# Kernel tuning notes

Measured on AMD Instinct MI355X. Metric: run time of the kernel, lower is better.

Reference implementation:

```python
import jax, jax.numpy as jnp
import numpy as np

B, S, E, H = 1, 4096, 768, 12
DH = E // H  # 64


def setup_inputs() -> dict:
    key = jax.random.key(0)
    ks = jax.random.split(key, 4)
    x = jax.random.normal(ks[0], (B, S, E), dtype=jnp.float32)
    mask = jnp.tril(jnp.ones((S, S), dtype=bool))  # causal mask, broadcast over B,H
    w_qkv = jax.random.normal(ks[1], (3 * E, E), dtype=jnp.float32) * 0.02
    b_qkv = jnp.zeros((3 * E,), dtype=jnp.float32)
    w_out = jax.random.normal(ks[2], (E, E), dtype=jnp.float32) * 0.02
    b_out = jnp.zeros((E,), dtype=jnp.float32)
    return {"x": x, "mask": mask, "w_qkv": w_qkv, "b_qkv": b_qkv,
            "w_out": w_out, "b_out": b_out}


def reference(x, mask, w_qkv, b_qkv, w_out, b_out):
    b, s, e = x.shape
    # qkv projection: torch Linear is x @ W^T + b
    qkv = x @ w_qkv.T + b_qkv                      # [B,S,3E]
    q, k, v = jnp.split(qkv, 3, axis=-1)           # each [B,S,E]
    def heads(t):
        return t.reshape(b, s, H, DH).transpose(0, 2, 1, 3)  # [B,H,S,Dh]
    q, k, v = heads(q), heads(k), heads(v)
    # NOTE: original module does NOT scale by 1/sqrt(head_dim)
    scores = jnp.einsum('bhqd,bhkd->bhqk', q, k)   # [B,H,S,S]
    scores = jnp.where(mask, scores, -jnp.inf)     # masked_fill(mask==0, -inf)
    probs = jax.nn.softmax(scores, axis=-1)        # dropout=0 (eval)
    attn = jnp.einsum('bhqk,bhkd->bhqd', probs, v) # [B,H,S,Dh]
    attn = attn.transpose(0, 2, 1, 3).reshape(b, s, e)
    return attn @ w_out.T + b_out
```

## Files before the change

### kernel.cpp

```cpp
#include <hip/hip_runtime.h>
#include <hip/hip_bf16.h>

#define S_LEN 4096
#define EMB   768
#define NH    12
#define DH    64
#define NCHUNK 4
#define CKL2   10

#define LOG2E 1.44269504088896f

#define NEG_BIG (-1e30f)

#define EXP2F(x) __builtin_amdgcn_exp2f(x)

using bf16x8 = __attribute__((ext_vector_type(8))) short;
using bf16x4 = __attribute__((ext_vector_type(4))) short;
using f32x4  = __attribute__((ext_vector_type(4))) float;

__device__ __forceinline__ short f2bf(float f) {
    __hip_bfloat16 h = __float2bfloat16(f);
    short s; __builtin_memcpy(&s, &h, 2); return s;
}
__device__ __forceinline__ float bf2f(short s) {
    __hip_bfloat16 h; __builtin_memcpy(&h, &s, 2);
    return __bfloat162float(h);
}

__device__ __forceinline__ unsigned pack_bf16_rh(float a, float b) {
    unsigned ua, ub;
    __builtin_memcpy(&ua, &a, 4);
    __builtin_memcpy(&ub, &b, 4);
    return __builtin_amdgcn_perm(ub + 0x8000u, ua + 0x8000u, 0x07060302u);
}

__device__ __forceinline__ void gld_lds16(const void* g, void* l) {
    __builtin_amdgcn_global_load_lds(
        (const __attribute__((address_space(1))) unsigned int*)g,
        (__attribute__((address_space(3))) unsigned int*)l, 16, 0, 0);
}

__device__ __forceinline__ void cvt8(const float* s, short* d, int i) {
    const float4 a = ((const float4*)s)[i * 2];
    const float4 b = ((const float4*)s)[i * 2 + 1];
    bf16x8 o;
    o[0] = f2bf(a.x); o[1] = f2bf(a.y); o[2] = f2bf(a.z); o[3] = f2bf(a.w);
    o[4] = f2bf(b.x); o[5] = f2bf(b.y); o[6] = f2bf(b.z); o[7] = f2bf(b.w);
    ((bf16x8*)d)[i] = o;
}

__global__ __launch_bounds__(256) void cvt_bf16(
    const float* __restrict__ s, short* __restrict__ d, int n8)
{
    const int i = blockIdx.x * 256 + threadIdx.x;
    if (i < n8) cvt8(s, d, i);
}

__global__ __launch_bounds__(256) void cvt3_bf16(
    const float* __restrict__ x,  short* __restrict__ xb,  int n8x,
    const float* __restrict__ wq, short* __restrict__ wqb, int n8q,
    const float* __restrict__ wo, short* __restrict__ wob, int n8o)
{
    int i = blockIdx.x * 256 + threadIdx.x;
    if (i < n8x) { cvt8(x, xb, i); return; }
    i -= n8x;
    if (i < n8q) { cvt8(wq, wqb, i); return; }
    i -= n8q;
    if (i < n8o) cvt8(wo, wob, i);
}

__global__ __launch_bounds__(256) void qkv_gemm(
    const short* __restrict__ Xb, const short* __restrict__ Wb,
    const float* __restrict__ Bias,
    short* __restrict__ Qw, short* __restrict__ Kw, short* __restrict__ Vt)
{
    __shared__ __align__(16) short SMEM[2 * 128 * 64];
    short* As = SMEM;
    short* Bs = SMEM + 128 * 64;

    const int m0 = blockIdx.x * 128;
    const int n0 = blockIdx.y * 128;
    const int t = threadIdx.x;
    const int lane = t & 63, wave = t >> 6;
    const int quad = lane >> 4, l16 = lane & 15;
    const int wm = (wave >> 1) * 64, wn = (wave & 1) * 64;
    const int srow = lane >> 3, scol = (lane & 7) * 8;

    f32x4 acc[4][4] = {};

    for (int k0 = 0; k0 < EMB; k0 += 64) {
        #pragma unroll
        for (int qd = 0; qd < 4; qd++) {
            const int chunk = wave * 4 + qd;
            const int row = chunk * 8 + srow;
            gld_lds16(&Xb[(size_t)(m0 + row) * EMB + k0 + scol], &As[chunk * 512]);
            gld_lds16(&Wb[(size_t)(n0 + row) * EMB + k0 + scol], &Bs[chunk * 512]);
        }
        __syncthreads();

        #pragma unroll
        for (int kb = 0; kb < 2; kb++) {
            bf16x8 af[4], bfr[4];
            #pragma unroll
            for (int i = 0; i < 4; i++)
                af[i] = *(const bf16x8*)&As[(wm + i * 16 + l16) * 64 + kb * 32 + quad * 8];
            #pragma unroll
            for (int j = 0; j < 4; j++)
                bfr[j] = *(const bf16x8*)&Bs[(wn + j * 16 + l16) * 64 + kb * 32 + quad * 8];
            #pragma unroll
            for (int i = 0; i < 4; i++)
                #pragma unroll
                for (int j = 0; j < 4; j++)
                    acc[i][j] = __builtin_amdgcn_mfma_f32_16x16x32_bf16(
                        af[i], bfr[j], acc[i][j], 0, 0, 0);
        }
        __syncthreads();
    }

    const int part = n0 / EMB;

    if (part < 2) {
        const float qs = (part == 0) ? LOG2E : 1.0f;
        #pragma unroll
        for (int j = 0; j < 4; j++) {
            const int n = n0 + wn + j * 16 + l16;
            const float bias = Bias[n];
            const int r768 = n % EMB;
            const int h = r768 >> 6, d = r768 & 63;
            short* dst = (part == 0) ? Qw : Kw;
            #pragma unroll
            for (int i = 0; i < 4; i++)
                #pragma unroll
                for (int r = 0; r < 4; r++) {
                    const int m = m0 + wm + i * 16 + quad * 4 + r;
                    dst[((size_t)h * S_LEN + m) * DH + d] =
                        f2bf((acc[i][j][r] + bias) * qs);
                }
        }
    } else {
        #pragma unroll
        for (int j = 0; j < 4; j++) {
            const int nl = wn + j * 16 + l16;
            const float bias = Bias[n0 + nl];
            #pragma unroll
            for (int i = 0; i < 4; i++) {
                short4 v;
                v.x = f2bf(acc[i][j][0] + bias);
                v.y = f2bf(acc[i][j][1] + bias);
                v.z = f2bf(acc[i][j][2] + bias);
                v.w = f2bf(acc[i][j][3] + bias);
                *(short4*)&SMEM[nl * 128 + wm + i * 16 + quad * 4] = v;
            }
        }
        __syncthreads();
        const int vrow0 = n0 - 2 * EMB;
        #pragma unroll
        for (int c = t; c < 2048; c += 256) {
            const int row = c >> 4, off = (c & 15) * 8;
            *(bf16x8*)&Vt[(size_t)(vrow0 + row) * S_LEN + m0 + off] =
                *(const bf16x8*)&SMEM[row * 128 + off];
        }
    }
}

__global__ __launch_bounds__(256, 4) void flash_partial(
    const short* __restrict__ Qw, const short* __restrict__ Kw,
    const short* __restrict__ Vt,
    short* __restrict__ Opart, float* __restrict__ Mpart,
    float* __restrict__ Lpart)
{
    const int qt = (gridDim.x - 1) - blockIdx.x;
    const int h  = blockIdx.y;
    const int kc = blockIdx.z;
    const int q0  = qt * 64;
    const int ks0 = kc << CKL2;
    if (ks0 > q0) return;
    const int KIT = (1 << CKL2) / 128;
    const int T  = q0 >> 7;
    const int nk = min(KIT, T - KIT * kc + 1);

    __shared__ __align__(16) short SMEM[128 * 64 + 64 * 128];
    short* Ks = SMEM;
    short* Vs = SMEM + 128 * 64;

    const int t = threadIdx.x;
    const int lane = t & 63, wave = t >> 6;
    const int quad = lane >> 4, l16 = lane & 15;
    const int qw0 = q0 + wave * 16;
    const int swk = (l16 & 7) << 4;
    const int swv = l16 << 4;

    const short* Kh = Kw + (size_t)h * S_LEN * DH;
    const short* Vh = Vt + (size_t)h * DH * S_LEN;

    const int krow = lane >> 3;
    const int kcol = ((lane & 7) ^ krow) << 3;
    const int vrow = lane >> 4;
    const int vsc  = lane & 15;

    bf16x8 qf[2];
    #pragma unroll
    for (int kb = 0; kb < 2; kb++)
        qf[kb] = *(const bf16x8*)
            &Qw[((size_t)h * S_LEN + qw0 + l16) * DH + kb * 32 + quad * 8];

    float m_i = NEG_BIG, l_i = 0.f;
    f32x4 o_acc[4] = {};

    for (int kt = 0; kt < nk; kt++) {
        const int k0 = ks0 + kt * 128;

        __syncthreads();
        #pragma unroll
        for (int i = 0; i < 4; i++) {
            const int ck = wave * 4 + i;
            const int rk = ck * 8 + krow;
            gld_lds16(&Kh[(size_t)(k0 + rk) * DH + kcol], &Ks[ck * 512]);
            const int rv = ck * 4 + vrow;
            const int vcol = (vsc ^ (rv & 15)) << 3;
            gld_lds16(&Vh[(size_t)rv * S_LEN + k0 + vcol], &Vs[ck * 512]);
        }
        __syncthreads();

        const bool maskn = (k0 + 127 > q0);
        #pragma unroll
        for (int sub = 0; sub < 2; sub++) {
            const int kbase = k0 + sub * 64;
            if (maskn && kbase > qw0 + 15) continue;

            f32x4 sfT[4] = {};
            __builtin_amdgcn_s_setprio(1);
            #pragma unroll
            for (int bb = 0; bb < 4; bb++) {
                const int row = (sub * 4 + bb) * 16 + l16;
                #pragma unroll
                for (int kb = 0; kb < 2; kb++) {
                    const bf16x8 kf = *(const bf16x8*)((const char*)Ks
                        + row * 128 + ((kb * 64 + quad * 16) ^ swk));
                    sfT[bb] = __builtin_amdgcn_mfma_f32_16x16x32_bf16(
                        kf, qf[kb], sfT[bb], 0, 0, 0);
                }
            }
            __builtin_amdgcn_s_setprio(0);

            const int qg = qw0 + l16;
            if (maskn) {
                #pragma unroll
                for (int bb = 0; bb < 4; bb++)
                    #pragma unroll
                    for (int r = 0; r < 4; r++)
                        if (kbase + bb * 16 + quad * 4 + r > qg)
                            sfT[bb][r] = NEG_BIG;
            }

            float mx = sfT[0][0];
            #pragma unroll
            for (int bb = 0; bb < 4; bb++)
                #pragma unroll
                for (int r = 0; r < 4; r++) mx = fmaxf(mx, sfT[bb][r]);
            mx = fmaxf(mx, __shfl_xor(mx, 16, 64));
            mx = fmaxf(mx, __shfl_xor(mx, 32, 64));
            if (!__all(mx <= m_i + 8.0f)) {
                const float mnew = fmaxf(m_i, mx);
                const float alpha = EXP2F(m_i - mnew);
                m_i = mnew;
                l_i *= alpha;
                #pragma unroll
                for (int db = 0; db < 4; db++) o_acc[db] *= alpha;
            }
            float rs = 0.f;
            #pragma unroll
            for (int bb = 0; bb < 4; bb++)
                #pragma unroll
                for (int r = 0; r < 4; r++) {
                    const float p = EXP2F(sfT[bb][r] - m_i);
                    sfT[bb][r] = p;
                    rs += p;
                }
            rs += __shfl_xor(rs, 16, 64);
            rs += __shfl_xor(rs, 32, 64);
            l_i += rs;

            __builtin_amdgcn_s_setprio(1);
            #pragma unroll
            for (int bp = 0; bp < 2; bp++) {
                int4 pv;
                pv.x = (int)pack_bf16_rh(sfT[2 * bp][0],     sfT[2 * bp][1]);
                pv.y = (int)pack_bf16_rh(sfT[2 * bp][2],     sfT[2 * bp][3]);
                pv.z = (int)pack_bf16_rh(sfT[2 * bp + 1][0], sfT[2 * bp + 1][1]);
                pv.w = (int)pack_bf16_rh(sfT[2 * bp + 1][2], sfT[2 * bp + 1][3]);
                const bf16x8 pf = __builtin_bit_cast(bf16x8, pv);
                const int colb = (sub * 2 + bp) * 64 + quad * 8;
                #pragma unroll
                for (int db = 0; db < 4; db++) {
                    const char* vb = (const char*)Vs + (db * 16 + l16) * 256;
                    const int2 lo2 = *(const int2*)(vb + (colb ^ swv));
                    const int2 hi2 = *(const int2*)(vb + ((colb + 32) ^ swv));
                    int4 vi; vi.x = lo2.x; vi.y = lo2.y; vi.z = hi2.x; vi.w = hi2.y;
                    o_acc[db] = __builtin_amdgcn_mfma_f32_16x16x32_bf16(
                        __builtin_bit_cast(bf16x8, vi), pf, o_acc[db], 0, 0, 0);
                }
            }
            __builtin_amdgcn_s_setprio(0);
        }
    }

    const size_t slab = ((size_t)h * NCHUNK + kc) * S_LEN;

    if (quad == 0) {
        const int q = qw0 + l16;
        Mpart[slab + q] = m_i;
        Lpart[slab + q] = l_i;
    }

    __syncthreads();
    #pragma unroll
    for (int db = 0; db < 4; db++) {
        short4 pk4;
        pk4.x = f2bf(o_acc[db][0]); pk4.y = f2bf(o_acc[db][1]);
        pk4.z = f2bf(o_acc[db][2]); pk4.w = f2bf(o_acc[db][3]);
        *(short4*)&SMEM[(wave * 16 + l16) * 72 + db * 16 + quad * 4] = pk4;
    }
    __syncthreads();
    #pragma unroll
    for (int c = t; c < 512; c += 256) {
        const int row = c >> 3, off = (c & 7) * 8;
        *(bf16x8*)&Opart[(slab + q0 + row) * DH + off] =
            *(const bf16x8*)&SMEM[row * 72 + off];
    }
}

__global__ __launch_bounds__(256) void flash_merge(
    const short* __restrict__ Opart, const float* __restrict__ Mpart,
    const float* __restrict__ Lpart, short* __restrict__ Ctx)
{
    const int row = blockIdx.x * 4 + (threadIdx.x >> 6);
    const int lane = threadIdx.x & 63;
    const int h = row >> 12, q = row & 4095;
    const int nc = (q >> CKL2) + 1;

    float mv[NCHUNK], lv[NCHUNK];
    float M = NEG_BIG;
    #pragma unroll
    for (int c = 0; c < NCHUNK; c++) {
        if (c < nc) {
            mv[c] = Mpart[((size_t)h * NCHUNK + c) * S_LEN + q];
            lv[c] = Lpart[((size_t)h * NCHUNK + c) * S_LEN + q];
            M = fmaxf(M, mv[c]);
        }
    }
    float L = 0.f, O = 0.f;
    #pragma unroll
    for (int c = 0; c < NCHUNK; c++) {
        if (c < nc) {
            const float w = EXP2F(mv[c] - M);
            L += w * lv[c];
            O += w * bf2f(Opart[(((size_t)h * NCHUNK + c) * S_LEN + q) * DH + lane]);
        }
    }
    const float inv = (L > 0.f) ? 1.0f / L : 0.f;
    Ctx[(size_t)q * EMB + h * DH + lane] = f2bf(O * inv);
}

__global__ __launch_bounds__(256) void flash_attn(
    const short* __restrict__ Qw, const short* __restrict__ Kw,
    const short* __restrict__ Vt, short* __restrict__ Ctx)
{
    __shared__ __align__(16) short Ks[128 * 64];
    __shared__ __align__(16) short Vs[64 * 128];
    __shared__ __align__(16) short Ps[4][32 * 128];

    const int h  = blockIdx.y;
    const int qt = (gridDim.x - 1) - blockIdx.x;
    const int q0 = qt * 128;
    const int t = threadIdx.x;
    const int lane = t & 63, wave = t >> 6;
    const int quad = lane >> 4, l16 = lane & 15;
    const int qw0 = q0 + wave * 32;

    bf16x8 qf[2][2];
    #pragma unroll
    for (int i = 0; i < 2; i++)
        #pragma unroll
        for (int kb = 0; kb < 2; kb++)
            qf[i][kb] = *(const bf16x8*)
                &Qw[((size_t)h * S_LEN + qw0 + i * 16 + l16) * DH + kb * 32 + quad * 8];

    float m_i[2][4], l_i[2][4];
    f32x4 o_acc[2][4] = {};
    #pragma unroll
    for (int i = 0; i < 2; i++)
        #pragma unroll
        for (int r = 0; r < 4; r++) { m_i[i][r] = NEG_BIG; l_i[i][r] = 0.f; }

    for (int kt = 0; kt <= qt; kt++) {
        const int k0 = kt * 128;
        __syncthreads();
        for (int c = t; c < 1024; c += 256) {
            const int row = c >> 3, cc = (c & 7) * 8;
            *(bf16x8*)&Ks[row * 64 + cc] =
                *(const bf16x8*)&Kw[((size_t)h * S_LEN + k0 + row) * DH + cc];
        }
        for (int c = t; c < 1024; c += 256) {
            const int row = c >> 4, cc = (c & 15) * 8;
            *(bf16x8*)&Vs[row * 128 + cc] =
                *(const bf16x8*)&Vt[((size_t)h * DH + row) * S_LEN + k0 + cc];
        }
        __syncthreads();

        f32x4 sf[2][8] = {};
        #pragma unroll
        for (int j = 0; j < 8; j++) {
            #pragma unroll
            for (int kb = 0; kb < 2; kb++) {
                const bf16x8 kf = *(const bf16x8*)
                    &Ks[(j * 16 + l16) * 64 + kb * 32 + quad * 8];
                #pragma unroll
                for (int i = 0; i < 2; i++)
                    sf[i][j] = __builtin_amdgcn_mfma_f32_16x16x32_bf16(
                        qf[i][kb], kf, sf[i][j], 0, 0, 0);
            }
        }

        const bool diag = (kt == qt);
        #pragma unroll
        for (int i = 0; i < 2; i++) {
            if (diag) {
                const int qbase = qw0 + i * 16 + quad * 4;
                const int kbase = k0 + l16;
                #pragma unroll
                for (int j = 0; j < 8; j++)
                    #pragma unroll
                    for (int r = 0; r < 4; r++)
                        if (kbase + j * 16 > qbase + r) sf[i][j][r] = NEG_BIG;
            }
            #pragma unroll
            for (int r = 0; r < 4; r++) {
                float mx = sf[i][0][r];
                #pragma unroll
                for (int j = 1; j < 8; j++) mx = fmaxf(mx, sf[i][j][r]);
                #pragma unroll
                for (int off = 1; off < 16; off <<= 1)
                    mx = fmaxf(mx, __shfl_xor(mx, off, 64));
                const float mnew = fmaxf(m_i[i][r], mx);
                const float alpha = EXP2F(m_i[i][r] - mnew);
                m_i[i][r] = mnew;
                float rs = 0.f;
                #pragma unroll
                for (int j = 0; j < 8; j++) {
                    const float p = EXP2F(sf[i][j][r] - mnew);
                    sf[i][j][r] = p;
                    rs += p;
                }
                #pragma unroll
                for (int off = 1; off < 16; off <<= 1)
                    rs += __shfl_xor(rs, off, 64);
                l_i[i][r] = l_i[i][r] * alpha + rs;
                #pragma unroll
                for (int db = 0; db < 4; db++) o_acc[i][db][r] *= alpha;
            }
            #pragma unroll
            for (int j = 0; j < 8; j++)
                #pragma unroll
                for (int r = 0; r < 4; r++)
                    Ps[wave][(i * 16 + quad * 4 + r) * 128 + j * 16 + l16] =
                        f2bf(sf[i][j][r]);
        }

        #pragma unroll
        for (int kb = 0; kb < 4; kb++) {
            bf16x8 pf[2];
            #pragma unroll
            for (int i = 0; i < 2; i++)
                pf[i] = *(const bf16x8*)
                    &Ps[wave][(i * 16 + l16) * 128 + kb * 32 + quad * 8];
            #pragma unroll
            for (int db = 0; db < 4; db++) {
                const bf16x8 vf = *(const bf16x8*)
                    &Vs[(db * 16 + l16) * 128 + kb * 32 + quad * 8];
                #pragma unroll
                for (int i = 0; i < 2; i++)
                    o_acc[i][db] = __builtin_amdgcn_mfma_f32_16x16x32_bf16(
                        pf[i], vf, o_acc[i][db], 0, 0, 0);
            }
        }
    }

    #pragma unroll
    for (int i = 0; i < 2; i++)
        #pragma unroll
        for (int r = 0; r < 4; r++) {
            const float li = l_i[i][r];
            const float inv = (li > 0.f) ? 1.0f / li : 0.f;
            const int m = qw0 + i * 16 + quad * 4 + r;
            #pragma unroll
            for (int db = 0; db < 4; db++) {
                const int d = db * 16 + l16;
                Ctx[(size_t)m * EMB + h * DH + d] = f2bf(o_acc[i][db][r] * inv);
            }
        }
}

__global__ __launch_bounds__(256) void out_gemm(
    const short* __restrict__ A, const short* __restrict__ Wb,
    const float* __restrict__ Bias, float* __restrict__ Out)
{
    __shared__ __align__(16) short As[128 * 64];
    __shared__ __align__(16) short Bs[128 * 64];

    const int m0 = blockIdx.x * 128;
    const int n0 = blockIdx.y * 128;
    const int t = threadIdx.x;
    const int lane = t & 63, wave = t >> 6;
    const int quad = lane >> 4, l16 = lane & 15;
    const int wm = (wave >> 1) * 64, wn = (wave & 1) * 64;
    const int srow = lane >> 3, scol = (lane & 7) * 8;

    f32x4 acc[4][4] = {};

    for (int k0 = 0; k0 < EMB; k0 += 64) {
        #pragma unroll
        for (int qd = 0; qd < 4; qd++) {
            const int chunk = wave * 4 + qd;
            const int row = chunk * 8 + srow;
            gld_lds16(&A [(size_t)(m0 + row) * EMB + k0 + scol], &As[chunk * 512]);
            gld_lds16(&Wb[(size_t)(n0 + row) * EMB + k0 + scol], &Bs[chunk * 512]);
        }
        __syncthreads();

        #pragma unroll
        for (int kb = 0; kb < 2; kb++) {
            bf16x8 af[4], bfr[4];
            #pragma unroll
            for (int i = 0; i < 4; i++)
                af[i] = *(const bf16x8*)&As[(wm + i * 16 + l16) * 64 + kb * 32 + quad * 8];
            #pragma unroll
            for (int j = 0; j < 4; j++)
                bfr[j] = *(const bf16x8*)&Bs[(wn + j * 16 + l16) * 64 + kb * 32 + quad * 8];
            #pragma unroll
            for (int i = 0; i < 4; i++)
                #pragma unroll
                for (int j = 0; j < 4; j++)
                    acc[i][j] = __builtin_amdgcn_mfma_f32_16x16x32_bf16(
                        af[i], bfr[j], acc[i][j], 0, 0, 0);
        }
        __syncthreads();
    }

    #pragma unroll
    for (int j = 0; j < 4; j++) {
        const int n = n0 + wn + j * 16 + l16;
        const float bias = Bias[n];
        #pragma unroll
        for (int i = 0; i < 4; i++)
            #pragma unroll
            for (int r = 0; r < 4; r++) {
                const int m = m0 + wm + i * 16 + quad * 4 + r;
                Out[(size_t)m * EMB + n] = acc[i][j][r] + bias;
            }
    }
}

extern "C" void kernel_launch(void* const* d_in, const int* in_sizes, int n_in,
                              void* d_out, int out_size, void* d_ws, size_t ws_size,
                              hipStream_t stream)
{
    (void)in_sizes; (void)n_in; (void)out_size;
    const float* x     = (const float*)d_in[0];
    const float* w_qkv = (const float*)d_in[2];
    const float* b_qkv = (const float*)d_in[3];
    const float* w_out = (const float*)d_in[4];
    const float* b_out = (const float*)d_in[5];
    float* out = (float*)d_out;

    char* ws = (char*)d_ws;
    const size_t SEG = (size_t)NH * S_LEN * DH * sizeof(short);
    short* Qw  = (short*)(ws);
    short* Kw  = (short*)(ws + SEG);
    short* Vt  = (short*)(ws + 2 * SEG);
    short* Ctx = (short*)(ws + 3 * SEG);
    const size_t OP_OFF = 4 * SEG;
    const size_t OP_SZ  = (size_t)NH * NCHUNK * S_LEN * DH * sizeof(short);
    const size_t ML_SZ  = (size_t)NH * NCHUNK * S_LEN * sizeof(float);
    short* Opart = (short*)(ws + OP_OFF);
    float* Mpart = (float*)(ws + OP_OFF + OP_SZ);
    float* Lpart = (float*)(ws + OP_OFF + OP_SZ + ML_SZ);
    const size_t need = OP_OFF + OP_SZ + 2 * ML_SZ;

    const int XN8 = (S_LEN * EMB) / 8;
    const int WQ8 = (3 * EMB * EMB) / 8;
    const int WO8 = (EMB * EMB) / 8;
    const size_t WO_BYTES = (size_t)EMB * EMB * sizeof(short);
    short* Xb    = (short*)(ws + OP_OFF);
    short* Wqkvb = (short*)(ws + OP_OFF + (size_t)XN8 * 8 * sizeof(short));
    const bool big = ws_size >= need + WO_BYTES;
    short* Woutb = big ? (short*)(ws + need) : (short*)(ws + OP_OFF);

    if (big) {
        const int tot8 = XN8 + WQ8 + WO8;
        cvt3_bf16<<<dim3((tot8 + 255) / 256), 256, 0, stream>>>(
            x, Xb, XN8, w_qkv, Wqkvb, WQ8, w_out, Woutb, WO8);
    } else {
        cvt_bf16<<<dim3((XN8 + 255) / 256), 256, 0, stream>>>(x, Xb, XN8);
        cvt_bf16<<<dim3((WQ8 + 255) / 256), 256, 0, stream>>>(w_qkv, Wqkvb, WQ8);
    }

    qkv_gemm<<<dim3(S_LEN / 128, (3 * EMB) / 128), 256, 0, stream>>>(
        Xb, Wqkvb, b_qkv, Qw, Kw, Vt);

    if (ws_size >= need) {
        flash_partial<<<dim3(S_LEN / 64, NH, NCHUNK), 256, 0, stream>>>(
            Qw, Kw, Vt, Opart, Mpart, Lpart);
        flash_merge<<<dim3(NH * S_LEN / 4), 256, 0, stream>>>(
            Opart, Mpart, Lpart, Ctx);
    } else {
        flash_attn<<<dim3(S_LEN / 128, NH), 256, 0, stream>>>(Qw, Kw, Vt, Ctx);
    }

    if (!big)
        cvt_bf16<<<dim3((WO8 + 255) / 256), 256, 0, stream>>>(w_out, Woutb, WO8);
    out_gemm<<<dim3(S_LEN / 128, EMB / 128), 256, 0, stream>>>(
        Ctx, Woutb, b_out, out);
}
```

Measured before the change: 254.4 us.

## Double-buffer K/V tiles, process full 128-key tile, fold row-sum into MFMA

Adds a two-stage LDS ping-pong so the next K/V tile loads asynchronously while the current one is computed, using explicit vmcnt waits and barriers. The two 64-key sub-iterations are merged into one 128-key softmax step, so the max and rescale work runs once per tile. The softmax row-sum is now produced by an extra MFMA against a ones vector instead of shuffle reductions, and packing uses v_cvt_pk_bf16_f32. LDS doubles and launch bounds drop to 2 waves per SIMD, which lowers occupancy and raises register pressure.

```diff
diff --git a/kernel.cpp b/kernel.cpp
--- a/kernel.cpp
+++ b/kernel.cpp
@@ -32,6 +32,12 @@
     __builtin_memcpy(&ua, &a, 4);
     __builtin_memcpy(&ub, &b, 4);
     return __builtin_amdgcn_perm(ub + 0x8000u, ua + 0x8000u, 0x07060302u);
+}
+
+__device__ __forceinline__ unsigned cvt_pk_bf16(float a, float b) {
+    unsigned r;
+    asm("v_cvt_pk_bf16_f32 %0, %1, %2" : "=v"(r) : "v"(a), "v"(b));
+    return r;
 }
 
 __device__ __forceinline__ void gld_lds16(const void* g, void* l) {
@@ -163,7 +169,7 @@
     }
 }
 
-__global__ __launch_bounds__(256, 4) void flash_partial(
+__global__ __launch_bounds__(256, 2) void flash_partial(
     const short* __restrict__ Qw, const short* __restrict__ Kw,
     const short* __restrict__ Vt,
     short* __restrict__ Opart, float* __restrict__ Mpart,
@@ -179,9 +185,7 @@
     const int T  = q0 >> 7;
     const int nk = min(KIT, T - KIT * kc + 1);
 
-    __shared__ __align__(16) short SMEM[128 * 64 + 64 * 128];
-    short* Ks = SMEM;
-    short* Vs = SMEM + 128 * 64;
+    __shared__ __align__(16) short SMEM[2 * 16384];
 
     const int t = threadIdx.x;
     const int lane = t & 63, wave = t >> 6;
@@ -204,93 +208,118 @@
         qf[kb] = *(const bf16x8*)
             &Qw[((size_t)h * S_LEN + qw0 + l16) * DH + kb * 32 + quad * 8];
 
-    float m_i = NEG_BIG, l_i = 0.f;
-    f32x4 o_acc[4] = {};
-
-    for (int kt = 0; kt < nk; kt++) {
-        const int k0 = ks0 + kt * 128;
-
-        __syncthreads();
+    bf16x8 vfc;
+    {
+        const short o1 = (l16 == 0) ? (short)0x3F80 : (short)0;
+        #pragma unroll
+        for (int c = 0; c < 8; c++) vfc[c] = o1;
+    }
+
+    auto stage = [&](int K0, int p) {
+        short* Ks = SMEM + p * 16384;
+        short* Vs = Ks + 8192;
         #pragma unroll
         for (int i = 0; i < 4; i++) {
             const int ck = wave * 4 + i;
             const int rk = ck * 8 + krow;
-            gld_lds16(&Kh[(size_t)(k0 + rk) * DH + kcol], &Ks[ck * 512]);
+            gld_lds16(&Kh[(size_t)(K0 + rk) * DH + kcol], &Ks[ck * 512]);
             const int rv = ck * 4 + vrow;
             const int vcol = (vsc ^ (rv & 15)) << 3;
-            gld_lds16(&Vh[(size_t)rv * S_LEN + k0 + vcol], &Vs[ck * 512]);
-        }
-        __syncthreads();
+            gld_lds16(&Vh[(size_t)rv * S_LEN + K0 + vcol], &Vs[ck * 512]);
+        }
+    };
+
+    stage(ks0, 0);
+
+    float m_i = NEG_BIG;
+    f32x4 o_acc[5] = {};
+
+    for (int kt = 0; kt < nk; kt++) {
+        const int k0 = ks0 + kt * 128;
+        const int p = kt & 1;
+        const short* Ks = SMEM + p * 16384;
+        const short* Vs = Ks + 8192;
+
+        __builtin_amdgcn_sched_barrier(0);
+        if (kt + 1 < nk) {
+            stage(k0 + 128, p ^ 1);
+            __builtin_amdgcn_sched_barrier(0);
+            asm volatile("s_waitcnt vmcnt(8)" ::: "memory");
+        } else {
+            asm volatile("s_waitcnt vmcnt(0)" ::: "memory");
+        }
+        __builtin_amdgcn_sched_barrier(0);
+        __builtin_amdgcn_s_barrier();
+        __builtin_amdgcn_sched_barrier(0);
 
         const bool maskn = (k0 + 127 > q0);
-        #pragma unroll
-        for (int sub = 0; sub < 2; sub++) {
-            const int kbase = k0 + sub * 64;
-            if (maskn && kbase > qw0 + 15) continue;
-
-            f32x4 sfT[4] = {};
-            __builtin_amdgcn_s_setprio(1);
-            #pragma unroll
-            for (int bb = 0; bb < 4; bb++) {
-                const int row = (sub * 4 + bb) * 16 + l16;
+        const bool do1 = !(maskn && (k0 + 64 > qw0 + 15));
+
+        f32x4 sfT[8];
+        __builtin_amdgcn_s_setprio(1);
+        #pragma unroll
+        for (int j = 0; j < 8; j++) {
+            if (j < 4 || do1) {
+                sfT[j] = f32x4{};
+                const int row = j * 16 + l16;
                 #pragma unroll
                 for (int kb = 0; kb < 2; kb++) {
                     const bf16x8 kf = *(const bf16x8*)((const char*)Ks
                         + row * 128 + ((kb * 64 + quad * 16) ^ swk));
-                    sfT[bb] = __builtin_amdgcn_mfma_f32_16x16x32_bf16(
-                        kf, qf[kb], sfT[bb], 0, 0, 0);
+                    sfT[j] = __builtin_amdgcn_mfma_f32_16x16x32_bf16(
+                        kf, qf[kb], sfT[j], 0, 0, 0);
                 }
             }
-            __builtin_amdgcn_s_setprio(0);
-
-            const int qg = qw0 + l16;
-            if (maskn) {
-                #pragma unroll
-                for (int bb = 0; bb < 4; bb++)
+        }
+        __builtin_amdgcn_s_setprio(0);
+
+        const int qg = qw0 + l16;
+        if (maskn) {
+            #pragma unroll
+            for (int j = 0; j < 8; j++)
+                if (j < 4 || do1) {
                     #pragma unroll
                     for (int r = 0; r < 4; r++)
-                        if (kbase + bb * 16 + quad * 4 + r > qg)
-                            sfT[bb][r] = NEG_BIG;
-            }
-
-            float mx = sfT[0][0];
-            #pragma unroll
-            for (int bb = 0; bb < 4; bb++)
-                #pragma unroll
-                for (int r = 0; r < 4; r++) mx = fmaxf(mx, sfT[bb][r]);
-            mx = fmaxf(mx, __shfl_xor(mx, 16, 64));
-            mx = fmaxf(mx, __shfl_xor(mx, 32, 64));
-            if (!__all(mx <= m_i + 8.0f)) {
-                const float mnew = fmaxf(m_i, mx);
-                const float alpha = EXP2F(m_i - mnew);
-                m_i = mnew;
-                l_i *= alpha;
-                #pragma unroll
-                for (int db = 0; db < 4; db++) o_acc[db] *= alpha;
-            }
-            float rs = 0.f;
-            #pragma unroll
-            for (int bb = 0; bb < 4; bb++)
-                #pragma unroll
-                for (int r = 0; r < 4; r++) {
-                    const float p = EXP2F(sfT[bb][r] - m_i);
-                    sfT[bb][r] = p;
-                    rs += p;
+                        if (k0 + j * 16 + quad * 4 + r > qg)
+                            sfT[j][r] = NEG_BIG;
                 }
-            rs += __shfl_xor(rs, 16, 64);
-            rs += __shfl_xor(rs, 32, 64);
-            l_i += rs;
-
-            __builtin_amdgcn_s_setprio(1);
-            #pragma unroll
-            for (int bp = 0; bp < 2; bp++) {
+        }
+
+        float mx = sfT[0][0];
+        #pragma unroll
+        for (int j = 0; j < 8; j++)
+            if (j < 4 || do1) {
+                #pragma unroll
+                for (int r = 0; r < 4; r++) mx = fmaxf(mx, sfT[j][r]);
+            }
+        mx = fmaxf(mx, __shfl_xor(mx, 16, 64));
+        mx = fmaxf(mx, __shfl_xor(mx, 32, 64));
+        if (!__all(mx <= m_i + 8.0f)) {
+            const float mnew = fmaxf(m_i, mx);
+            const float alpha = EXP2F(m_i - mnew);
+            m_i = mnew;
+            #pragma unroll
+            for (int db = 0; db < 5; db++) o_acc[db] *= alpha;
+        }
+        #pragma unroll
+        for (int j = 0; j < 8; j++)
+            if (j < 4 || do1) {
+                #pragma unroll
+                for (int r = 0; r < 4; r++)
+                    sfT[j][r] = EXP2F(sfT[j][r] - m_i);
+            }
+
+        __builtin_amdgcn_s_setprio(1);
+        #pragma unroll
+        for (int bp = 0; bp < 4; bp++) {
+            if (bp < 2 || do1) {
                 int4 pv;
-                pv.x = (int)pack_bf16_rh(sfT[2 * bp][0],     sfT[2 * bp][1]);
-                pv.y = (int)pack_bf16_rh(sfT[2 * bp][2],     sfT[2 * bp][3]);
-                pv.z = (int)pack_bf16_rh(sfT[2 * bp + 1][0], sfT[2 * bp + 1][1]);
-                pv.w = (int)pack_bf16_rh(sfT[2 * bp + 1][2], sfT[2 * bp + 1][3]);
+                pv.x = (int)cvt_pk_bf16(sfT[2 * bp][0],     sfT[2 * bp][1]);
+                pv.y = (int)cvt_pk_bf16(sfT[2 * bp][2],     sfT[2 * bp][3]);
+                pv.z = (int)cvt_pk_bf16(sfT[2 * bp + 1][0], sfT[2 * bp + 1][1]);
+                pv.w = (int)cvt_pk_bf16(sfT[2 * bp + 1][2], sfT[2 * bp + 1][3]);
                 const bf16x8 pf = __builtin_bit_cast(bf16x8, pv);
-                const int colb = (sub * 2 + bp) * 64 + quad * 8;
+                const int colb = bp * 64 + quad * 8;
                 #pragma unroll
                 for (int db = 0; db < 4; db++) {
                     const char* vb = (const char*)Vs + (db * 16 + l16) * 256;
@@ -300,9 +329,14 @@
                     o_acc[db] = __builtin_amdgcn_mfma_f32_16x16x32_bf16(
                         __builtin_bit_cast(bf16x8, vi), pf, o_acc[db], 0, 0, 0);
                 }
-            }
-            __builtin_amdgcn_s_setprio(0);
-        }
+                o_acc[4] = __builtin_amdgcn_mfma_f32_16x16x32_bf16(
+                    vfc, pf, o_acc[4], 0, 0, 0);
+            }
+        }
+        __builtin_amdgcn_s_setprio(0);
+
+        __builtin_amdgcn_sched_barrier(0);
+        __builtin_amdgcn_s_barrier();
     }
 
     const size_t slab = ((size_t)h * NCHUNK + kc) * S_LEN;
@@ -310,7 +344,7 @@
     if (quad == 0) {
         const int q = qw0 + l16;
         Mpart[slab + q] = m_i;
-        Lpart[slab + q] = l_i;
+        Lpart[slab + q] = o_acc[4][0];
     }
 
     __syncthreads();
```

Result: slower. 265.1 us (+4.2%).

## Process two 16-row query tiles per wave and compute row sums via MFMA

Applied to the files above, without the earlier changes.

Each flash_partial block now covers 128 query rows, with each wave handling 32 rows as two 16-row tiles. Every K/V fragment loaded from LDS is reused across both tiles, which halves K/V staging traffic per query and the grid size. The softmax row sum is computed by an extra MFMA against a ones-column vector instead of shuffle reductions. P is packed to bf16 with a hardware convert instruction in place of the manual round-half perm trick. The costs are more registers (launch bounds drop from 4 to 3 blocks per CU), fewer blocks to fill the GPU, and the risk that the l computed from bf16-rounded P differs slightly from the fp32 sum.

```diff
diff --git a/kernel.cpp b/kernel.cpp
--- a/kernel.cpp
+++ b/kernel.cpp
@@ -27,11 +27,10 @@
     return __bfloat162float(h);
 }
 
-__device__ __forceinline__ unsigned pack_bf16_rh(float a, float b) {
-    unsigned ua, ub;
-    __builtin_memcpy(&ua, &a, 4);
-    __builtin_memcpy(&ub, &b, 4);
-    return __builtin_amdgcn_perm(ub + 0x8000u, ua + 0x8000u, 0x07060302u);
+__device__ __forceinline__ unsigned cvt_pk_bf16(float a, float b) {
+    unsigned r;
+    asm("v_cvt_pk_bf16_f32 %0, %1, %2" : "=v"(r) : "v"(a), "v"(b));
+    return r;
 }
 
 __device__ __forceinline__ void gld_lds16(const void* g, void* l) {
@@ -163,7 +162,7 @@
     }
 }
 
-__global__ __launch_bounds__(256, 4) void flash_partial(
+__global__ __launch_bounds__(256, 3) void flash_partial(
     const short* __restrict__ Qw, const short* __restrict__ Kw,
     const short* __restrict__ Vt,
     short* __restrict__ Opart, float* __restrict__ Mpart,
@@ -172,12 +171,11 @@
     const int qt = (gridDim.x - 1) - blockIdx.x;
     const int h  = blockIdx.y;
     const int kc = blockIdx.z;
-    const int q0  = qt * 64;
+    const int q0  = qt * 128;
     const int ks0 = kc << CKL2;
     if (ks0 > q0) return;
     const int KIT = (1 << CKL2) / 128;
-    const int T  = q0 >> 7;
-    const int nk = min(KIT, T - KIT * kc + 1);
+    const int nk = min(KIT, (q0 >> 7) - KIT * kc + 1);
 
     __shared__ __align__(16) short SMEM[128 * 64 + 64 * 128];
     short* Ks = SMEM;
@@ -186,7 +184,7 @@
     const int t = threadIdx.x;
     const int lane = t & 63, wave = t >> 6;
     const int quad = lane >> 4, l16 = lane & 15;
-    const int qw0 = q0 + wave * 16;
+    const int qw0 = q0 + wave * 32;
     const int swk = (l16 & 7) << 4;
     const int swv = l16 << 4;
 
@@ -198,14 +196,23 @@
     const int vrow = lane >> 4;
     const int vsc  = lane & 15;
 
-    bf16x8 qf[2];
-    #pragma unroll
-    for (int kb = 0; kb < 2; kb++)
-        qf[kb] = *(const bf16x8*)
-            &Qw[((size_t)h * S_LEN + qw0 + l16) * DH + kb * 32 + quad * 8];
-
-    float m_i = NEG_BIG, l_i = 0.f;
-    f32x4 o_acc[4] = {};
+    bf16x8 qf[2][2];
+    #pragma unroll
+    for (int i = 0; i < 2; i++)
+        #pragma unroll
+        for (int kb = 0; kb < 2; kb++)
+            qf[i][kb] = *(const bf16x8*)
+                &Qw[((size_t)h * S_LEN + qw0 + i * 16 + l16) * DH + kb * 32 + quad * 8];
+
+    bf16x8 vfc;
+    {
+        const short o1 = (l16 == 0) ? (short)0x3F80 : (short)0;
+        #pragma unroll
+        for (int c = 0; c < 8; c++) vfc[c] = o1;
+    }
+
+    float m_i[2] = {NEG_BIG, NEG_BIG};
+    f32x4 o_acc[2][5] = {};
 
     for (int kt = 0; kt < nk; kt++) {
         const int k0 = ks0 + kt * 128;
@@ -226,70 +233,86 @@
         #pragma unroll
         for (int sub = 0; sub < 2; sub++) {
             const int kbase = k0 + sub * 64;
-            if (maskn && kbase > qw0 + 15) continue;
-
-            f32x4 sfT[4] = {};
+            if (maskn && kbase > qw0 + 31) continue;
+            const bool a0 = !(maskn && kbase > qw0 + 15);
+
+            f32x4 sfT[2][4];
             __builtin_amdgcn_s_setprio(1);
             #pragma unroll
             for (int bb = 0; bb < 4; bb++) {
                 const int row = (sub * 4 + bb) * 16 + l16;
-                #pragma unroll
-                for (int kb = 0; kb < 2; kb++) {
-                    const bf16x8 kf = *(const bf16x8*)((const char*)Ks
+                bf16x8 kf[2];
+                #pragma unroll
+                for (int kb = 0; kb < 2; kb++)
+                    kf[kb] = *(const bf16x8*)((const char*)Ks
                         + row * 128 + ((kb * 64 + quad * 16) ^ swk));
-                    sfT[bb] = __builtin_amdgcn_mfma_f32_16x16x32_bf16(
-                        kf, qf[kb], sfT[bb], 0, 0, 0);
+                sfT[1][bb] = f32x4{};
+                #pragma unroll
+                for (int kb = 0; kb < 2; kb++)
+                    sfT[1][bb] = __builtin_amdgcn_mfma_f32_16x16x32_bf16(
+                        kf[kb], qf[1][kb], sfT[1][bb], 0, 0, 0);
+                if (a0) {
+                    sfT[0][bb] = f32x4{};
+                    #pragma unroll
+                    for (int kb = 0; kb < 2; kb++)
+                        sfT[0][bb] = __builtin_amdgcn_mfma_f32_16x16x32_bf16(
+                            kf[kb], qf[0][kb], sfT[0][bb], 0, 0, 0);
                 }
             }
             __builtin_amdgcn_s_setprio(0);
 
-            const int qg = qw0 + l16;
             if (maskn) {
+                #pragma unroll
+                for (int i = 0; i < 2; i++) {
+                    if (i == 0 && !a0) continue;
+                    const int qg = qw0 + i * 16 + l16;
+                    #pragma unroll
+                    for (int bb = 0; bb < 4; bb++)
+                        #pragma unroll
+                        for (int r = 0; r < 4; r++)
+                            if (kbase + bb * 16 + quad * 4 + r > qg)
+                                sfT[i][bb][r] = NEG_BIG;
+                }
+            }
+
+            #pragma unroll
+            for (int i = 0; i < 2; i++) {
+                if (i == 0 && !a0) continue;
+                float mx = sfT[i][0][0];
+                #pragma unroll
+                for (int bb = 0; bb < 4; bb++)
+                    #pragma unroll
+                    for (int r = 0; r < 4; r++) mx = fmaxf(mx, sfT[i][bb][r]);
+                mx = fmaxf(mx, __shfl_xor(mx, 16, 64));
+                mx = fmaxf(mx, __shfl_xor(mx, 32, 64));
+                if (!__all(mx <= m_i[i] + 8.0f)) {
+                    const float mnew = fmaxf(m_i[i], mx);
+                    const float alpha = EXP2F(m_i[i] - mnew);
+                    m_i[i] = mnew;
+                    #pragma unroll
+                    for (int db = 0; db < 5; db++) o_acc[i][db] *= alpha;
+                }
                 #pragma unroll
                 for (int bb = 0; bb < 4; bb++)
                     #pragma unroll
                     for (int r = 0; r < 4; r++)
-                        if (kbase + bb * 16 + quad * 4 + r > qg)
-                            sfT[bb][r] = NEG_BIG;
-            }
-
-            float mx = sfT[0][0];
-            #pragma unroll
-            for (int bb = 0; bb < 4; bb++)
-                #pragma unroll
-                for (int r = 0; r < 4; r++) mx = fmaxf(mx, sfT[bb][r]);
-            mx = fmaxf(mx, __shfl_xor(mx, 16, 64));
-            mx = fmaxf(mx, __shfl_xor(mx, 32, 64));
-            if (!__all(mx <= m_i + 8.0f)) {
-                const float mnew = fmaxf(m_i, mx);
-                const float alpha = EXP2F(m_i - mnew);
-                m_i = mnew;
-                l_i *= alpha;
-                #pragma unroll
-                for (int db = 0; db < 4; db++) o_acc[db] *= alpha;
-            }
-            float rs = 0.f;
-            #pragma unroll
-            for (int bb = 0; bb < 4; bb++)
-                #pragma unroll
-                for (int r = 0; r < 4; r++) {
-                    const float p = EXP2F(sfT[bb][r] - m_i);
-                    sfT[bb][r] = p;
-                    rs += p;
+                        sfT[i][bb][r] = EXP2F(sfT[i][bb][r] - m_i[i]);
+            }
+
+            __builtin_amdgcn_s_setprio(1);
+            #pragma unroll
+            for (int bp = 0; bp < 2; bp++) {
+                bf16x8 pf[2];
+                #pragma unroll
+                for (int i = 0; i < 2; i++) {
+                    if (i == 0 && !a0) continue;
+                    int4 pv;
+                    pv.x = (int)cvt_pk_bf16(sfT[i][2 * bp][0],     sfT[i][2 * bp][1]);
+                    pv.y = (int)cvt_pk_bf16(sfT[i][2 * bp][2],     sfT[i][2 * bp][3]);
+                    pv.z = (int)cvt_pk_bf16(sfT[i][2 * bp + 1][0], sfT[i][2 * bp + 1][1]);
+                    pv.w = (int)cvt_pk_bf16(sfT[i][2 * bp + 1][2], sfT[i][2 * bp + 1][3]);
+                    pf[i] = __builtin_bit_cast(bf16x8, pv);
                 }
-            rs += __shfl_xor(rs, 16, 64);
-            rs += __shfl_xor(rs, 32, 64);
-            l_i += rs;
-
-            __builtin_amdgcn_s_setprio(1);
-            #pragma unroll
-            for (int bp = 0; bp < 2; bp++) {
-                int4 pv;
-                pv.x = (int)pack_bf16_rh(sfT[2 * bp][0],     sfT[2 * bp][1]);
-                pv.y = (int)pack_bf16_rh(sfT[2 * bp][2],     sfT[2 * bp][3]);
-                pv.z = (int)pack_bf16_rh(sfT[2 * bp + 1][0], sfT[2 * bp + 1][1]);
-                pv.w = (int)pack_bf16_rh(sfT[2 * bp + 1][2], sfT[2 * bp + 1][3]);
-                const bf16x8 pf = __builtin_bit_cast(bf16x8, pv);
                 const int colb = (sub * 2 + bp) * 64 + quad * 8;
                 #pragma unroll
                 for (int db = 0; db < 4; db++) {
@@ -297,9 +320,18 @@
                     const int2 lo2 = *(const int2*)(vb + (colb ^ swv));
                     const int2 hi2 = *(const int2*)(vb + ((colb + 32) ^ swv));
                     int4 vi; vi.x = lo2.x; vi.y = lo2.y; vi.z = hi2.x; vi.w = hi2.y;
-                    o_acc[db] = __builtin_amdgcn_mfma_f32_16x16x32_bf16(
-                        __builtin_bit_cast(bf16x8, vi), pf, o_acc[db], 0, 0, 0);
+                    const bf16x8 vf = __builtin_bit_cast(bf16x8, vi);
+                    o_acc[1][db] = __builtin_amdgcn_mfma_f32_16x16x32_bf16(
+                        vf, pf[1], o_acc[1][db], 0, 0, 0);
+                    if (a0)
+                        o_acc[0][db] = __builtin_amdgcn_mfma_f32_16x16x32_bf16(
+                            vf, pf[0], o_acc[0][db], 0, 0, 0);
                 }
+                o_acc[1][4] = __builtin_amdgcn_mfma_f32_16x16x32_bf16(
+                    vfc, pf[1], o_acc[1][4], 0, 0, 0);
+                if (a0)
+                    o_acc[0][4] = __builtin_amdgcn_mfma_f32_16x16x32_bf16(
+                        vfc, pf[0], o_acc[0][4], 0, 0, 0);
             }
             __builtin_amdgcn_s_setprio(0);
         }
@@ -307,23 +339,27 @@
 
     const size_t slab = ((size_t)h * NCHUNK + kc) * S_LEN;
 
-    if (quad == 0) {
-        const int q = qw0 + l16;
-        Mpart[slab + q] = m_i;
-        Lpart[slab + q] = l_i;
-    }
+    #pragma unroll
+    for (int i = 0; i < 2; i++)
+        if (quad == 0) {
+            const int q = qw0 + i * 16 + l16;
+            Mpart[slab + q] = m_i[i];
+            Lpart[slab + q] = o_acc[i][4][0];
+        }
 
     __syncthreads();
     #pragma unroll
-    for (int db = 0; db < 4; db++) {
-        short4 pk4;
-        pk4.x = f2bf(o_acc[db][0]); pk4.y = f2bf(o_acc[db][1]);
-        pk4.z = f2bf(o_acc[db][2]); pk4.w = f2bf(o_acc[db][3]);
-        *(short4*)&SMEM[(wave * 16 + l16) * 72 + db * 16 + quad * 4] = pk4;
-    }
+    for (int i = 0; i < 2; i++)
+        #pragma unroll
+        for (int db = 0; db < 4; db++) {
+            short4 pk4;
+            pk4.x = f2bf(o_acc[i][db][0]); pk4.y = f2bf(o_acc[i][db][1]);
+            pk4.z = f2bf(o_acc[i][db][2]); pk4.w = f2bf(o_acc[i][db][3]);
+            *(short4*)&SMEM[(wave * 32 + i * 16 + l16) * 72 + db * 16 + quad * 4] = pk4;
+        }
     __syncthreads();
     #pragma unroll
-    for (int c = t; c < 512; c += 256) {
+    for (int c = t; c < 1024; c += 256) {
         const int row = c >> 3, off = (c & 7) * 8;
         *(bf16x8*)&Opart[(slab + q0 + row) * DH + off] =
             *(const bf16x8*)&SMEM[row * 72 + off];
@@ -609,7 +645,7 @@
         Xb, Wqkvb, b_qkv, Qw, Kw, Vt);
 
     if (ws_size >= need) {
-        flash_partial<<<dim3(S_LEN / 64, NH, NCHUNK), 256, 0, stream>>>(
+        flash_partial<<<dim3(S_LEN / 128, NH, NCHUNK), 256, 0, stream>>>(
             Qw, Kw, Vt, Opart, Mpart, Lpart);
         flash_merge<<<dim3(NH * S_LEN / 4), 256, 0, stream>>>(
             Opart, Mpart, Lpart, Ctx);
```

New measurement: 251.2 us. Within noise of the previous version (-1.2%).
